# Kernel optimization log

Hardware: AMD Instinct MI355X
Metric: run time of the kernel (lower is better)

The kernel has to match this reference:

```python
import jax, jax.numpy as jnp
import numpy as np


def sage_conv(x, src, dst, n, W_l, b_l, W_r):
    # PyG SAGEConv (mean aggr): out = lin_l(mean_{j in N(i)} x_j) + lin_r(x_i)
    msg = x[src]                                            # [E, d_in] gather
    s = jax.ops.segment_sum(msg, dst, num_segments=n)       # [N, d_in]
    cnt = jax.ops.segment_sum(jnp.ones((src.shape[0], 1), x.dtype), dst, num_segments=n)
    mean = s / jnp.maximum(cnt, 1.0)
    return mean @ W_l.T + b_l + x @ W_r.T


def setup_inputs() -> dict:
    key = jax.random.key(0)
    ks = jax.random.split(key, 12)
    N, E, D = 200000, 6400000, 128
    x = jax.random.normal(ks[0], (N, D), dtype=jnp.float32)
    edge_index = jax.random.randint(ks[1], (2, E), 0, N, dtype=jnp.int64)

    def lin(k, dout, din, scale=None):
        s = scale if scale is not None else 1.0 / np.sqrt(din)
        return jax.random.uniform(k, (dout, din), jnp.float32, -s, s)

    return {
        "x": x,
        "edge_index": edge_index,
        "W1_l": lin(ks[2], 64, D), "b1_l": jnp.zeros((64,), jnp.float32), "W1_r": lin(ks[3], 64, D),
        "W2_l": lin(ks[4], 32, 64), "b2_l": jnp.zeros((32,), jnp.float32), "W2_r": lin(ks[5], 32, 64),
        "W3_l": lin(ks[6], 16, 32), "b3_l": jnp.zeros((16,), jnp.float32), "W3_r": lin(ks[7], 16, 32),
        "W_reg": lin(ks[8], 1, 16), "b_reg": jnp.zeros((1,), jnp.float32),
        "W_cls": lin(ks[9], 1, 16), "b_cls": jnp.zeros((1,), jnp.float32),
    }


def reference(x, edge_index, W1_l, b1_l, W1_r, W2_l, b2_l, W2_r, W3_l, b3_l, W3_r,
              W_reg, b_reg, W_cls, b_cls):
    # eval mode: dropout is identity
    n = x.shape[0]
    src, dst = edge_index[0], edge_index[1]
    h = jax.nn.relu(sage_conv(x, src, dst, n, W1_l, b1_l, W1_r))
    h = jax.nn.relu(sage_conv(h, src, dst, n, W2_l, b2_l, W2_r))
    h = jax.nn.relu(sage_conv(h, src, dst, n, W3_l, b3_l, W3_r))
    reg = (h @ W_reg.T + b_reg)[:, 0]
    cls = (h @ W_cls.T + b_cls)[:, 0]
    return (reg, cls)
```

## Files before the change

kernel.cpp:

```cpp
#include <hip/hip_runtime.h>


typedef __bf16 bf16x8 __attribute__((ext_vector_type(8)));
typedef float  f32x4  __attribute__((ext_vector_type(4)));

__device__ __forceinline__ unsigned short f2bf_rne(float f) {
    unsigned int u = __float_as_uint(f);
    u = (u + 0x7FFFu + ((u >> 16) & 1u)) >> 16;
    return (unsigned short)u;
}

__device__ __forceinline__ void bfacc(float4& a, const uint2 q) {
    a.x += __uint_as_float(q.x << 16);
    a.y += __uint_as_float(q.x & 0xFFFF0000u);
    a.z += __uint_as_float(q.y << 16);
    a.w += __uint_as_float(q.y & 0xFFFF0000u);
}

__global__ __launch_bounds__(256) void k_wprep(const float* __restrict__ W1l,
                                               const float* __restrict__ W1r,
                                               const float* __restrict__ W2l,
                                               const float* __restrict__ W2r,
                                               const float* __restrict__ W3l,
                                               const float* __restrict__ W3r,
                                               __bf16* __restrict__ O) {
    int i = blockIdx.x * 256 + threadIdx.x;
    const float *Wl, *Wr; __bf16* base; int idx, n, DIN, DOUT;
    if (i < 8192)       { Wl = W1l; Wr = W1r; base = O;         idx = i;         n = 8192; DIN = 128; DOUT = 64; }
    else if (i < 10240) { Wl = W2l; Wr = W2r; base = O + 24576; idx = i - 8192;  n = 2048; DIN = 64;  DOUT = 32; }
    else if (i < 10752) { Wl = W3l; Wr = W3r; base = O + 30720; idx = i - 10240; n = 512;  DIN = 32;  DOUT = 16; }
    else return;
    int c = idx / DIN, k = idx % DIN;
    int pos = ((k >> 3) * DOUT + c) * 8 + (k & 7);
    float wl = Wl[idx], wr = Wr[idx];
    __bf16 h = (__bf16)wr;
    base[pos]         = (__bf16)wl;
    base[n + pos]     = h;
    base[2 * n + pos] = (__bf16)(wr - (float)h);
}


__global__ __launch_bounds__(256) void k_bcount(const int* __restrict__ dst, int E, int N,
                                                int* __restrict__ bcnt) {
    __shared__ int h[256];
    const int tid = threadIdx.x;
    h[tid] = 0;
    __syncthreads();
    const int stride = gridDim.x * 256;
    for (int i = blockIdx.x * 256 + tid; i < E; i += stride) {
        int d = dst[i];
        d = d < 0 ? 0 : (d >= N ? N - 1 : d);
        atomicAdd(&h[d >> 10], 1);
    }
    __syncthreads();
    if (h[tid]) atomicAdd(&bcnt[tid], h[tid]);
}

__global__ __launch_bounds__(256) void k_bscan(const int* __restrict__ bcnt,
                                               int* __restrict__ boff,
                                               int* __restrict__ bcur, int NBK, int E) {
    __shared__ int sd[256];
    const int tid = threadIdx.x;
    bcur[tid] = 0;
    int v = (tid < NBK) ? bcnt[tid] : 0;
    sd[tid] = v; __syncthreads();
    for (int off = 1; off < 256; off <<= 1) {
        int t = (tid >= off) ? sd[tid - off] : 0;
        __syncthreads();
        sd[tid] += t;
        __syncthreads();
    }
    if (tid < NBK) boff[tid] = sd[tid] - v;
    if (tid == 0) boff[NBK] = E;
}

#define BTILE 4096
__global__ __launch_bounds__(256) void k_bucket(const int* __restrict__ src,
                                                const int* __restrict__ dst, int E, int N,
                                                const int* __restrict__ boff,
                                                int* __restrict__ bcur,
                                                int* __restrict__ T, int NBK) {
    __shared__ int cnt[256], cnt2[256], lofs[256], gbase[256], boffs[256], sd[256];
    __shared__ int2 staged[BTILE];
    const int tid = threadIdx.x;
    const int tb = blockIdx.x * BTILE;
    const int tn = min(BTILE, E - tb);
    cnt[tid] = 0; cnt2[tid] = 0;
    boffs[tid] = (tid < NBK) ? boff[tid] : 0;
    __syncthreads();
    for (int i = tid; i < tn; i += 256) {
        int d = dst[tb + i];
        d = d < 0 ? 0 : (d >= N ? N - 1 : d);
        atomicAdd(&cnt[d >> 10], 1);
    }
    __syncthreads();
    int v = cnt[tid];
    sd[tid] = v; __syncthreads();
    for (int off = 1; off < 256; off <<= 1) {
        int t = (tid >= off) ? sd[tid - off] : 0;
        __syncthreads();
        sd[tid] += t;
        __syncthreads();
    }
    lofs[tid] = sd[tid] - v;
    if (v > 0 && tid < NBK) gbase[tid] = atomicAdd(&bcur[tid], v);
    __syncthreads();
    for (int i = tid; i < tn; i += 256) {
        int d = dst[tb + i];
        d = d < 0 ? 0 : (d >= N ? N - 1 : d);
        int s = src[tb + i];
        s = s < 0 ? 0 : (s >= N ? N - 1 : s);
        int b = d >> 10;
        int r = atomicAdd(&cnt2[b], 1);
        staged[lofs[b] + r] = make_int2(s, d);
    }
    __syncthreads();
    for (int i = tid; i < tn; i += 256) {
        int2 p = staged[i];
        int b = p.y >> 10;
        T[(size_t)boffs[b] + gbase[b] + (i - lofs[b])] = ((p.y & 1023) << 18) | p.x;
    }
}

__global__ __launch_bounds__(1024) void k_csr(const int* __restrict__ T,
                                              const int* __restrict__ boff,
                                              int* __restrict__ rowptr,
                                              int* __restrict__ adj, int N, int E) {
    __shared__ int hist[1024];
    __shared__ int sc[1024];
    const int tid = threadIdx.x;
    const int b = blockIdx.x;
    const int node0 = b << 10;
    hist[tid] = 0;
    __syncthreads();
    const int beg = boff[b], end = boff[b + 1];
    for (int i = beg + tid; i < end; i += 1024)
        atomicAdd(&hist[((unsigned)T[i]) >> 18], 1);
    __syncthreads();
    int v = hist[tid];
    sc[tid] = v;
    __syncthreads();
    for (int off = 1; off < 1024; off <<= 1) {
        int t = (tid >= off) ? sc[tid - off] : 0;
        __syncthreads();
        sc[tid] += t;
        __syncthreads();
    }
    const int excl = beg + sc[tid] - v;
    const int n = node0 + tid;
    if (n < N) rowptr[n] = excl;
    if (b == 0 && tid == 0) rowptr[N] = E;
    hist[tid] = excl;
    __syncthreads();
    for (int i = beg + tid; i < end; i += 1024) {
        unsigned p = (unsigned)T[i];
        int pos = atomicAdd(&hist[p >> 18], 1);
        adj[pos] = (int)(p & 0x3FFFFu);
    }
}

template<int DIN, int DOUT>
__global__ __launch_bounds__(256) void proj_mfma(const float* __restrict__ H,
                                                 const __bf16* __restrict__ Wlb,
                                                 const __bf16* __restrict__ Wrh,
                                                 const __bf16* __restrict__ Wrl,
                                                 const float* __restrict__ bias,
                                                 unsigned short* __restrict__ Pl,
                                                 float* __restrict__ R, int N) {
    constexpr int COLT = DOUT / 16;
    const int wave = threadIdx.x >> 6, lane = threadIdx.x & 63;
    const int quad = lane >> 4, l16 = lane & 15;
    const int n0 = (blockIdx.x * 4 + wave) * 16;
    int arow = n0 + l16;
    if (arow >= N) arow = N - 1;
    const float* hrow = H + (size_t)arow * DIN;

    f32x4 zero = {0.f, 0.f, 0.f, 0.f};
    f32x4 accP[COLT], accR[COLT];
    #pragma unroll
    for (int t = 0; t < COLT; ++t) { accP[t] = zero; accR[t] = zero; }

    for (int k0 = 0; k0 < DIN; k0 += 32) {
        const float* hp = hrow + k0 + quad * 8;
        float4 h0 = *(const float4*)hp;
        float4 h1 = *(const float4*)(hp + 4);
        float hv[8] = {h0.x, h0.y, h0.z, h0.w, h1.x, h1.y, h1.z, h1.w};
        bf16x8 ahi, alo;
        #pragma unroll
        for (int j = 0; j < 8; ++j) {
            __bf16 hb = (__bf16)hv[j];
            ahi[j] = hb;
            alo[j] = (__bf16)(hv[j] - (float)hb);
        }
        const int u = (k0 >> 3) + quad;
        #pragma unroll
        for (int t = 0; t < COLT; ++t) {
            const int c = t * 16 + l16;
            const int wpos = (u * DOUT + c) * 8;
            bf16x8 bl  = *(const bf16x8*)&Wlb[wpos];
            bf16x8 brh = *(const bf16x8*)&Wrh[wpos];
            bf16x8 brl = *(const bf16x8*)&Wrl[wpos];
            accP[t] = __builtin_amdgcn_mfma_f32_16x16x32_bf16(ahi, bl,  accP[t], 0, 0, 0);
            accR[t] = __builtin_amdgcn_mfma_f32_16x16x32_bf16(ahi, brh, accR[t], 0, 0, 0);
            accR[t] = __builtin_amdgcn_mfma_f32_16x16x32_bf16(ahi, brl, accR[t], 0, 0, 0);
            accR[t] = __builtin_amdgcn_mfma_f32_16x16x32_bf16(alo, brh, accR[t], 0, 0, 0);
        }
    }
    #pragma unroll
    for (int t = 0; t < COLT; ++t) {
        const int c = t * 16 + l16;
        const float bc = bias[c];
        #pragma unroll
        for (int r = 0; r < 4; ++r) {
            int node = n0 + quad * 4 + r;
            if (node < N) {
                Pl[(size_t)node * DOUT + c] = f2bf_rne(accP[t][r]);
                R[(size_t)node * DOUT + c] = accR[t][r] + bc;
            }
        }
    }
}

template<int D, int DP>
__global__ __launch_bounds__(256, 8) void gather_proj(const unsigned short* __restrict__ P,
                                                      const int* __restrict__ rowptr,
                                                      const int* __restrict__ adj,
                                                      const float* __restrict__ Rres,
                                                      const __bf16* __restrict__ Wlb,
                                                      const __bf16* __restrict__ Wrh,
                                                      const __bf16* __restrict__ Wrl,
                                                      const float* __restrict__ bias,
                                                      unsigned short* __restrict__ Pout,
                                                      float* __restrict__ Rout, int N) {
    constexpr int L   = D / 4;
    constexpr int S   = 64 / L;
    constexpr int M   = 4;
    constexpr int NPW = S * M;
    constexpr int NPB = NPW * 4;
    constexpr int SP  = D + 4;
    constexpr int COLT = DP / 16;
    __shared__ __align__(16) float hstage[NPB * SP];

    const int wave = threadIdx.x >> 6, lane = threadIdx.x & 63;
    const int sub = lane / L, cl = lane % L;
    const uint2* __restrict__ P2 = (const uint2*)P;
    const f32x4* __restrict__ R4 = (const f32x4*)Rres;
    const int base = blockIdx.x * NPB + wave * NPW + sub;

    #pragma unroll 1
    for (int m = 0; m < M; ++m) {
        const int n = base + m * S;
        const int lrow = wave * NPW + sub + m * S;
        f32x4 o = {0.f, 0.f, 0.f, 0.f};
        if (n < N) {
            int beg = rowptr[n], end = rowptr[n + 1];
            float4 a0 = {0, 0, 0, 0}, a1 = {0, 0, 0, 0}, a2 = {0, 0, 0, 0}, a3 = {0, 0, 0, 0};
            int j = beg;
            while (j < end && (j & 3)) { bfacc(a0, P2[adj[j] * L + cl]); ++j; }
            for (; j + 8 <= end; j += 8) {
                int4 sA = *(const int4*)(adj + j);
                int4 sB = *(const int4*)(adj + j + 4);
                uint2 p0 = P2[sA.x * L + cl];
                uint2 p1 = P2[sA.y * L + cl];
                uint2 p2 = P2[sA.z * L + cl];
                uint2 p3 = P2[sA.w * L + cl];
                uint2 p4 = P2[sB.x * L + cl];
                uint2 p5 = P2[sB.y * L + cl];
                uint2 p6 = P2[sB.z * L + cl];
                uint2 p7 = P2[sB.w * L + cl];
                bfacc(a0, p0); bfacc(a1, p1); bfacc(a2, p2); bfacc(a3, p3);
                bfacc(a0, p4); bfacc(a1, p5); bfacc(a2, p6); bfacc(a3, p7);
            }
            if (j + 4 <= end) {
                int4 sA = *(const int4*)(adj + j);
                bfacc(a0, P2[sA.x * L + cl]);
                bfacc(a1, P2[sA.y * L + cl]);
                bfacc(a2, P2[sA.z * L + cl]);
                bfacc(a3, P2[sA.w * L + cl]);
                j += 4;
            }
            for (; j < end; ++j) bfacc(a0, P2[adj[j] * L + cl]);
            int deg = end - beg;
            float inv = deg > 0 ? 1.0f / (float)deg : 0.0f;
            f32x4 r = R4[(size_t)n * L + cl];
            o.x = fmaxf((a0.x + a1.x + a2.x + a3.x) * inv + r.x, 0.0f);
            o.y = fmaxf((a0.y + a1.y + a2.y + a3.y) * inv + r.y, 0.0f);
            o.z = fmaxf((a0.z + a1.z + a2.z + a3.z) * inv + r.z, 0.0f);
            o.w = fmaxf((a0.w + a1.w + a2.w + a3.w) * inv + r.w, 0.0f);
        }
        *(f32x4*)&hstage[lrow * SP + cl * 4] = o;
    }
    __syncthreads();

    const int quad = lane >> 4, l16 = lane & 15;
    f32x4 zero = {0.f, 0.f, 0.f, 0.f};
    #pragma unroll
    for (int tile = 0; tile < NPB / 64; ++tile) {
        const int trow0 = wave * NPW + tile * 16;
        f32x4 accP[COLT], accR[COLT];
        #pragma unroll
        for (int t = 0; t < COLT; ++t) { accP[t] = zero; accR[t] = zero; }
        #pragma unroll
        for (int k0 = 0; k0 < D; k0 += 32) {
            const int kk = k0 + quad * 8;
            const float* hp = &hstage[(trow0 + l16) * SP + kk];
            f32x4 h0 = *(const f32x4*)hp;
            f32x4 h1 = *(const f32x4*)(hp + 4);
            float hv[8] = {h0.x, h0.y, h0.z, h0.w, h1.x, h1.y, h1.z, h1.w};
            bf16x8 ahi, alo;
            #pragma unroll
            for (int j = 0; j < 8; ++j) {
                __bf16 hb = (__bf16)hv[j];
                ahi[j] = hb;
                alo[j] = (__bf16)(hv[j] - (float)hb);
            }
            const int u = (k0 >> 3) + quad;
            #pragma unroll
            for (int t = 0; t < COLT; ++t) {
                const int c = t * 16 + l16;
                const int wpos = (u * DP + c) * 8;
                bf16x8 bl  = *(const bf16x8*)&Wlb[wpos];
                bf16x8 brh = *(const bf16x8*)&Wrh[wpos];
                bf16x8 brl = *(const bf16x8*)&Wrl[wpos];
                accP[t] = __builtin_amdgcn_mfma_f32_16x16x32_bf16(ahi, bl,  accP[t], 0, 0, 0);
                accR[t] = __builtin_amdgcn_mfma_f32_16x16x32_bf16(ahi, brh, accR[t], 0, 0, 0);
                accR[t] = __builtin_amdgcn_mfma_f32_16x16x32_bf16(ahi, brl, accR[t], 0, 0, 0);
                accR[t] = __builtin_amdgcn_mfma_f32_16x16x32_bf16(alo, brh, accR[t], 0, 0, 0);
            }
        }
        #pragma unroll
        for (int t = 0; t < COLT; ++t) {
            const int c = t * 16 + l16;
            const float bc = bias[c];
            #pragma unroll
            for (int r = 0; r < 4; ++r) {
                int node = blockIdx.x * NPB + trow0 + quad * 4 + r;
                if (node < N) {
                    Pout[(size_t)node * DP + c] = f2bf_rne(accP[t][r]);
                    Rout[(size_t)node * DP + c] = accR[t][r] + bc;
                }
            }
        }
    }
}


template<int DOUT> struct GatherCfg {
    static constexpr int L   = DOUT / 4;
    static constexpr int S   = 64 / L;
    static constexpr int M   = 4;
    static constexpr int NPW = S * M;
    static constexpr int NPB = NPW * 4;
};

template<int DOUT>
__global__ __launch_bounds__(256, 8) void gather_head(const unsigned short* __restrict__ P,
                                                      const int* __restrict__ rowptr,
                                                      const int* __restrict__ adj,
                                                      const float* __restrict__ Rres, int N,
                                                      const float* __restrict__ Wreg,
                                                      const float* __restrict__ breg,
                                                      const float* __restrict__ Wcls,
                                                      const float* __restrict__ bcls,
                                                      float* __restrict__ out) {
    using C = GatherCfg<DOUT>;
    constexpr int L = C::L, S = C::S, M = C::M;
    constexpr int NPW = C::NPW, NPB = C::NPB;
    const int wave = threadIdx.x >> 6, lane = threadIdx.x & 63;
    const int sub = lane / L, cl = lane % L;
    const uint2* __restrict__ P2 = (const uint2*)P;
    const float4* __restrict__ R4 = (const float4*)Rres;
    const int base = blockIdx.x * NPB + wave * NPW + sub;
    #pragma unroll 1
    for (int m = 0; m < M; ++m) {
        int n = base + m * S;
        if (n >= N) continue;
        int beg = rowptr[n], end = rowptr[n + 1];
        float4 a0 = {0, 0, 0, 0}, a1 = {0, 0, 0, 0}, a2 = {0, 0, 0, 0}, a3 = {0, 0, 0, 0};
        int j = beg;
        while (j < end && (j & 3)) { bfacc(a0, P2[adj[j] * L + cl]); ++j; }
        for (; j + 8 <= end; j += 8) {
            int4 sA = *(const int4*)(adj + j);
            int4 sB = *(const int4*)(adj + j + 4);
            uint2 p0 = P2[sA.x * L + cl];
            uint2 p1 = P2[sA.y * L + cl];
            uint2 p2 = P2[sA.z * L + cl];
            uint2 p3 = P2[sA.w * L + cl];
            uint2 p4 = P2[sB.x * L + cl];
            uint2 p5 = P2[sB.y * L + cl];
            uint2 p6 = P2[sB.z * L + cl];
            uint2 p7 = P2[sB.w * L + cl];
            bfacc(a0, p0); bfacc(a1, p1); bfacc(a2, p2); bfacc(a3, p3);
            bfacc(a0, p4); bfacc(a1, p5); bfacc(a2, p6); bfacc(a3, p7);
        }
        if (j + 4 <= end) {
            int4 sA = *(const int4*)(adj + j);
            bfacc(a0, P2[sA.x * L + cl]);
            bfacc(a1, P2[sA.y * L + cl]);
            bfacc(a2, P2[sA.z * L + cl]);
            bfacc(a3, P2[sA.w * L + cl]);
            j += 4;
        }
        for (; j < end; ++j) bfacc(a0, P2[adj[j] * L + cl]);
        int deg = end - beg;
        float inv = deg > 0 ? 1.0f / (float)deg : 0.0f;
        float4 r = R4[(size_t)n * L + cl];
        float4 o;
        o.x = fmaxf((a0.x + a1.x + a2.x + a3.x) * inv + r.x, 0.0f);
        o.y = fmaxf((a0.y + a1.y + a2.y + a3.y) * inv + r.y, 0.0f);
        o.z = fmaxf((a0.z + a1.z + a2.z + a3.z) * inv + r.z, 0.0f);
        o.w = fmaxf((a0.w + a1.w + a2.w + a3.w) * inv + r.w, 0.0f);
        float4 wr = ((const float4*)Wreg)[cl];
        float4 wc = ((const float4*)Wcls)[cl];
        float pr = o.x * wr.x + o.y * wr.y + o.z * wr.z + o.w * wr.w;
        float pc = o.x * wc.x + o.y * wc.y + o.z * wc.z + o.w * wc.w;
        pr += __shfl_xor(pr, 1); pr += __shfl_xor(pr, 2);
        pc += __shfl_xor(pc, 1); pc += __shfl_xor(pc, 2);
        if (cl == 0) {
            out[n] = pr + breg[0];
            out[(size_t)N + n] = pc + bcls[0];
        }
    }
}

extern "C" void kernel_launch(void* const* d_in, const int* in_sizes, int n_in,
                              void* d_out, int out_size, void* d_ws, size_t ws_size,
                              hipStream_t stream) {
    const float* x    = (const float*)d_in[0];
    const int*   ei   = (const int*)d_in[1];
    const float* W1l  = (const float*)d_in[2];
    const float* b1l  = (const float*)d_in[3];
    const float* W1r  = (const float*)d_in[4];
    const float* W2l  = (const float*)d_in[5];
    const float* b2l  = (const float*)d_in[6];
    const float* W2r  = (const float*)d_in[7];
    const float* W3l  = (const float*)d_in[8];
    const float* b3l  = (const float*)d_in[9];
    const float* W3r  = (const float*)d_in[10];
    const float* Wreg = (const float*)d_in[11];
    const float* breg = (const float*)d_in[12];
    const float* Wcls = (const float*)d_in[13];
    const float* bcls = (const float*)d_in[14];

    const int N = in_sizes[0] / 128;
    const int E = in_sizes[1] / 2;
    const int* src = ei;
    const int* dst = ei + E;

    char* ws = (char*)d_ws;
    size_t off = 0;
    auto alloc = [&](size_t bytes) -> void* {
        void* p = ws + off;
        off += (bytes + 255) & ~(size_t)255;
        return p;
    };
    int*   rowptr = (int*)alloc((size_t)(N + 1) * 4);
    int*   bcnt   = (int*)alloc(1024);
    int*   bcur   = (int*)alloc(1024);
    int*   boff   = (int*)alloc(1028);
    int*   adj    = (int*)alloc((size_t)E * 4);
    __bf16* W16   = (__bf16*)alloc(32256 * 2);
    unsigned short* A1 = (unsigned short*)alloc((size_t)N * 64 * 2);
    unsigned short* A2 = (unsigned short*)alloc((size_t)N * 32 * 2);
    float* B      = (float*)alloc((size_t)N * 64 * 4);
    float* C      = (float*)alloc((size_t)N * 32 * 4);
    float* D      = (float*)alloc((size_t)N * 16 * 4);
    int*   T      = (int*)B;
    unsigned short* A3 = A1;

    const int NBK = (N + 1023) >> 10;

    k_wprep<<<42, 256, 0, stream>>>(W1l, W1r, W2l, W2r, W3l, W3r, W16);

    hipMemsetAsync(bcnt, 0, 1024, stream);
    k_bcount<<<1024, 256, 0, stream>>>(dst, E, N, bcnt);
    k_bscan<<<1, 256, 0, stream>>>(bcnt, boff, bcur, NBK, E);
    k_bucket<<<(E + BTILE - 1) / BTILE, 256, 0, stream>>>(src, dst, E, N, boff, bcur, T, NBK);
    k_csr<<<NBK, 1024, 0, stream>>>(T, boff, rowptr, adj, N, E);

    const int PB = 64;

    proj_mfma<128, 64><<<(N + PB - 1) / PB, 256, 0, stream>>>(
        x, W16, W16 + 8192, W16 + 16384, b1l, A1, B, N);
    gather_proj<64, 32><<<(N + 63) / 64, 256, 0, stream>>>(
        A1, rowptr, adj, B, W16 + 24576, W16 + 26624, W16 + 28672, b2l, A2, C, N);
    gather_proj<32, 16><<<(N + 127) / 128, 256, 0, stream>>>(
        A2, rowptr, adj, C, W16 + 30720, W16 + 31232, W16 + 31744, b3l, A3, D, N);
    constexpr int G16 = GatherCfg<16>::NPB;
    gather_head<16><<<(N + G16 - 1) / G16, 256, 0, stream>>>(
        A3, rowptr, adj, D, N, Wreg, breg, Wcls, bcls, (float*)d_out);
}
```

Measured before the change: 695.3 us.

## Sort nodes by degree within each block to balance gather work across lanes

Adds an in-block counting sort of nodes by in-degree (a histogram plus a prefix scan in shared memory). The gather loops then assign nodes to wave sub-groups in sorted order, so the sub-groups sharing a wave have similar neighbor counts and less SIMD divergence. Results are written back to each node's original slot. The cost is several extra __syncthreads, shared-memory atomics, and extra rowptr reads per block.

```diff
diff --git a/kernel.cpp b/kernel.cpp
--- a/kernel.cpp
+++ b/kernel.cpp
@@ -15,6 +15,39 @@
     a.y += __uint_as_float(q.x & 0xFFFF0000u);
     a.z += __uint_as_float(q.y << 16);
     a.w += __uint_as_float(q.y & 0xFFFF0000u);
+}
+
+template<int NPB_>
+__device__ __forceinline__ void degree_sort(const int* __restrict__ rowptr,
+                                            int block_base, int N,
+                                            unsigned short* slid,
+                                            int* dh, int* dsc) {
+    const int tid = threadIdx.x;
+    if (tid < 128) dh[tid] = 0;
+    __syncthreads();
+    int dg = 0;
+    if (tid < NPB_) {
+        int n = block_base + tid;
+        if (n < N) dg = min(rowptr[n + 1] - rowptr[n], 127);
+        atomicAdd(&dh[dg], 1);
+    }
+    __syncthreads();
+    if (tid < 128) dsc[tid] = dh[tid];
+    __syncthreads();
+    for (int off = 1; off < 128; off <<= 1) {
+        int t = 0;
+        if (tid < 128 && tid >= off) t = dsc[tid - off];
+        __syncthreads();
+        if (tid < 128) dsc[tid] += t;
+        __syncthreads();
+    }
+    if (tid < 128) dsc[tid] -= dh[tid];
+    __syncthreads();
+    if (tid < NPB_) {
+        int pos = atomicAdd(&dsc[dg], 1);
+        slid[pos] = (unsigned short)tid;
+    }
+    __syncthreads();
 }
 
 __global__ __launch_bounds__(256) void k_wprep(const float* __restrict__ W1l,
@@ -240,17 +273,22 @@
     constexpr int SP  = D + 4;
     constexpr int COLT = DP / 16;
     __shared__ __align__(16) float hstage[NPB * SP];
+    __shared__ unsigned short slid[NPB];
+    __shared__ int dh[128], dsc[128];
 
     const int wave = threadIdx.x >> 6, lane = threadIdx.x & 63;
     const int sub = lane / L, cl = lane % L;
     const uint2* __restrict__ P2 = (const uint2*)P;
     const f32x4* __restrict__ R4 = (const f32x4*)Rres;
-    const int base = blockIdx.x * NPB + wave * NPW + sub;
+    const int bb = blockIdx.x * NPB;
+
+    degree_sort<NPB>(rowptr, bb, N, slid, dh, dsc);
 
     #pragma unroll 1
     for (int m = 0; m < M; ++m) {
-        const int n = base + m * S;
-        const int lrow = wave * NPW + sub + m * S;
+        const int rank = wave * NPW + m * S + sub;
+        const int lid = slid[rank];
+        const int n = bb + lid;
         f32x4 o = {0.f, 0.f, 0.f, 0.f};
         if (n < N) {
             int beg = rowptr[n], end = rowptr[n + 1];
@@ -288,7 +326,7 @@
             o.z = fmaxf((a0.z + a1.z + a2.z + a3.z) * inv + r.z, 0.0f);
             o.w = fmaxf((a0.w + a1.w + a2.w + a3.w) * inv + r.w, 0.0f);
         }
-        *(f32x4*)&hstage[lrow * SP + cl * 4] = o;
+        *(f32x4*)&hstage[lid * SP + cl * 4] = o;
     }
     __syncthreads();
 
@@ -334,7 +372,7 @@
             const float bc = bias[c];
             #pragma unroll
             for (int r = 0; r < 4; ++r) {
-                int node = blockIdx.x * NPB + trow0 + quad * 4 + r;
+                int node = bb + trow0 + quad * 4 + r;
                 if (node < N) {
                     Pout[(size_t)node * DP + c] = f2bf_rne(accP[t][r]);
                     Rout[(size_t)node * DP + c] = accR[t][r] + bc;
@@ -366,14 +404,20 @@
     using C = GatherCfg<DOUT>;
     constexpr int L = C::L, S = C::S, M = C::M;
     constexpr int NPW = C::NPW, NPB = C::NPB;
+    __shared__ unsigned short slid[NPB];
+    __shared__ int dh[128], dsc[128];
     const int wave = threadIdx.x >> 6, lane = threadIdx.x & 63;
     const int sub = lane / L, cl = lane % L;
     const uint2* __restrict__ P2 = (const uint2*)P;
     const float4* __restrict__ R4 = (const float4*)Rres;
-    const int base = blockIdx.x * NPB + wave * NPW + sub;
+    const int bb = blockIdx.x * NPB;
+
+    degree_sort<NPB>(rowptr, bb, N, slid, dh, dsc);
+
     #pragma unroll 1
     for (int m = 0; m < M; ++m) {
-        int n = base + m * S;
+        const int rank = wave * NPW + m * S + sub;
+        const int n = bb + slid[rank];
         if (n >= N) continue;
         int beg = rowptr[n], end = rowptr[n + 1];
         float4 a0 = {0, 0, 0, 0}, a1 = {0, 0, 0, 0}, a2 = {0, 0, 0, 0}, a3 = {0, 0, 0, 0};
```

Result: slower. 712.7 us (+2.5%).
